# Performance work log

Measured on AMD Instinct MI355X. Metric: run time of the kernel, lower is better.

## Reference

```python
import jax, jax.numpy as jnp
import numpy as np

B, N, V, T = 16, 1024, 4096, 8


def _lsa(cost):
    """Jonker-Volgenant linear sum assignment on a square [n,n] cost matrix.
    Returns (row_ind, col_ind) minimizing cost[row, col].sum(). Equivalent to
    scipy.optimize.linear_sum_assignment for square matrices."""
    n = cost.shape[0]
    INF = np.inf
    u = np.zeros(n + 1)
    v = np.zeros(n + 1)
    p = np.zeros(n + 1, dtype=np.int64)    # p[j] = row assigned to column j (1-based)
    way = np.zeros(n + 1, dtype=np.int64)
    for i in range(1, n + 1):
        p[0] = i
        j0 = 0
        minv = np.full(n + 1, INF)
        used = np.zeros(n + 1, dtype=bool)
        while True:
            used[j0] = True
            i0 = p[j0]
            free = ~used
            free[0] = False
            cur = cost[i0 - 1, :] - u[i0] - v[1:]
            upd = free[1:] & (cur < minv[1:])
            minv[1:][upd] = cur[upd]
            way[1:][upd] = j0
            j1 = int(np.argmin(np.where(free[1:], minv[1:], INF))) + 1
            delta = minv[j1]
            u[p[used]] += delta
            v[used] -= delta
            minv[~used] -= delta
            j0 = j1
            if p[j0] == 0:
                break
        while j0:
            j1 = way[j0]
            p[j0] = p[j1]
            j0 = j1
    col_of_row = np.empty(n, dtype=np.int64)
    for j in range(1, n + 1):
        col_of_row[p[j] - 1] = j - 1
    return np.arange(n), col_of_row


def _compute_assignment(lp_np, gt_np, types_np, mask_np):
    """For each (sample, node_type) group of masked nodes, Hungarian-match
    positions to gt tokens. Returns flat (batch_idx, pos_idx, tok_idx) of all
    matched pairs. Mirrors the original type-wise padded loop (k==1 is identity)."""
    Bn = lp_np.shape[0]
    b_l, p_l, t_l = [], [], []
    for t in np.unique(types_np):
        for b in range(Bn):
            idx = np.nonzero((types_np[b] == t) & mask_np[b])[0]
            k = idx.size
            if k == 0:
                continue
            g = gt_np[b, idx]
            if k == 1:
                r = np.zeros(1, dtype=np.int64)
                c = np.zeros(1, dtype=np.int64)
            else:
                cost = -lp_np[b, idx][:, g]  # [k, k]
                r, c = _lsa(cost)
            b_l.append(np.full(k, b, dtype=np.int64))
            p_l.append(idx[r])
            t_l.append(g[c])
    return np.concatenate(b_l), np.concatenate(p_l), np.concatenate(t_l)


def setup_inputs() -> dict:
    key = jax.random.key(0)
    k1, k2, k3, k4 = jax.random.split(key, 4)
    logits = jax.random.normal(k1, (B, N, V), dtype=jnp.float32)
    gt_tokens = jax.random.randint(k2, (B, N), 0, V)
    node_types = jax.random.randint(k3, (B, N), 0, T)
    mask_positions = jax.random.randint(k4, (B, N), 0, 2).astype(bool)
    return {"logits": logits, "gt_tokens": gt_tokens,
            "node_types": node_types, "mask_positions": mask_positions}


def reference(logits, gt_tokens, node_types, mask_positions):
    # Dense log-softmax over vocab (the memory-bound bulk of the op).
    log_probs = jax.nn.log_softmax(logits, axis=-1)
    # Assignment is computed on detached values (matches .detach() in original).
    b_idx, p_idx, t_idx = _compute_assignment(
        np.asarray(jax.lax.stop_gradient(log_probs)),
        np.asarray(gt_tokens), np.asarray(node_types), np.asarray(mask_positions))
    total = b_idx.shape[0]  # total matched (masked) tokens
    sel = log_probs[jnp.asarray(b_idx), jnp.asarray(p_idx), jnp.asarray(t_idx)]
    # avg_loss = sum_b(loss_per_sample*count)/total_count == sum of matched NLL / total
    return -sel.sum() / jnp.asarray(total, sel.dtype)
```

## Files before the change

kernel.cpp:

```cpp
#include <hip/hip_runtime.h>
#include <math.h>

#define BB 16
#define NN 1024
#define VV 4096
#define TT 8
#define NG (BB*TT)
#define KMAX 124
#define STRIDE 124
#define LSEROWS 8

__device__ __forceinline__ float wave_sum(float v){
  #pragma unroll
  for (int off = 32; off; off >>= 1) v += __shfl_down(v, off);
  return v;
}

__device__ __forceinline__ unsigned fkey(float f){
  unsigned b = __float_as_uint(f);
  return b ^ ((unsigned)((int)b >> 31) | 0x80000000u);
}
__device__ __forceinline__ float inv_fkey(unsigned u){
  unsigned b = (u & 0x80000000u) ? (u ^ 0x80000000u) : ~u;
  return __uint_as_float(b);
}

__device__ __forceinline__ unsigned dpp_min64(unsigned x){
  unsigned t;
  t = (unsigned)__builtin_amdgcn_update_dpp(-1, (int)x, 0x111, 0xF, 0xF, false); x = x < t ? x : t;
  t = (unsigned)__builtin_amdgcn_update_dpp(-1, (int)x, 0x112, 0xF, 0xF, false); x = x < t ? x : t;
  t = (unsigned)__builtin_amdgcn_update_dpp(-1, (int)x, 0x114, 0xF, 0xF, false); x = x < t ? x : t;
  t = (unsigned)__builtin_amdgcn_update_dpp(-1, (int)x, 0x118, 0xF, 0xF, false); x = x < t ? x : t;
  t = (unsigned)__builtin_amdgcn_update_dpp(-1, (int)x, 0x142, 0xF, 0xF, false); x = x < t ? x : t;
  t = (unsigned)__builtin_amdgcn_update_dpp(-1, (int)x, 0x143, 0xF, 0xF, false); x = x < t ? x : t;
  return x;
}

__device__ __forceinline__ void lse_load(const float4* __restrict__ x, int lane,
                                         float4 (&v)[16]){
  #pragma unroll
  for (int i = 0; i < 16; i++) v[i] = x[lane + 64*i];
}
__device__ __forceinline__ float lse_reduce(const float4 (&v)[16]){
  float m = -INFINITY;
  #pragma unroll
  for (int i = 0; i < 16; i++)
    m = fmaxf(m, fmaxf(fmaxf(v[i].x, v[i].y), fmaxf(v[i].z, v[i].w)));
  #pragma unroll
  for (int off = 32; off; off >>= 1) m = fmaxf(m, __shfl_xor(m, off));
  float s = 0.f;
  #pragma unroll
  for (int i = 0; i < 16; i++)
    s += __expf(v[i].x - m) + __expf(v[i].y - m)
       + __expf(v[i].z - m) + __expf(v[i].w - m);
  #pragma unroll
  for (int off = 32; off; off >>= 1) s += __shfl_xor(s, off);
  return m + __logf(s);
}

__global__ __launch_bounds__(64) void k_main(const float* __restrict__ logits,
                                             const int* __restrict__ types,
                                             const int* __restrict__ gt,
                                             const unsigned char* __restrict__ raw,
                                             int* __restrict__ kcnt,
                                             float* __restrict__ gval,
                                             float* __restrict__ lse){
  int lane = threadIdx.x;

  if (blockIdx.x >= NG){
    int rbase = (blockIdx.x - NG) * LSEROWS;
    uchar4 pv = ((const uchar4*)raw)[lane];
    bool bool_layout = (__ballot((pv.y | pv.z | pv.w) != 0) != 0ull);
    const int* rawi = (const int*)raw;
    unsigned mb = 0;
    #pragma unroll
    for (int r = 0; r < LSEROWS; r++){
      int mv = bool_layout ? (int)raw[rbase + r] : rawi[rbase + r];
      mb |= (mv != 0) ? (1u << r) : 0u;
    }
    if (lane == 0){
      #pragma unroll
      for (int r = 0; r < LSEROWS; r++)
        if (!(mb & (1u << r))) lse[rbase + r] = 0.f;
    }
    if (mb == 0) return;

    float4 A[16], Bf[16];
    int rA = __ffs(mb) - 1;
    unsigned rem = mb & ~(1u << rA);
    lse_load((const float4*)(logits + (size_t)(rbase + rA) * VV), lane, A);
    while (true){
      int rB = rem ? (__ffs(rem) - 1) : -1;
      if (rB >= 0){
        rem &= ~(1u << rB);
        lse_load((const float4*)(logits + (size_t)(rbase + rB) * VV), lane, Bf);
      }
      float la = lse_reduce(A);
      if (lane == 0) lse[rbase + rA] = la;
      if (rB < 0) break;
      int rC = rem ? (__ffs(rem) - 1) : -1;
      if (rC >= 0){
        rem &= ~(1u << rC);
        lse_load((const float4*)(logits + (size_t)(rbase + rC) * VV), lane, A);
      }
      float lb = lse_reduce(Bf);
      if (lane == 0) lse[rbase + rB] = lb;
      if (rC < 0) break;
      rA = rC;
    }
    return;
  }

  __shared__ float Cm[KMAX*STRIDE];
  __shared__ float u_l[KMAX+1];
  __shared__ int   p_l[KMAX+1];
  __shared__ int   way_l[KMAX+1];
  __shared__ int   rowown[KMAX];
  __shared__ int   listA[KMAX];
  __shared__ int   listB[KMAX];
  int g = blockIdx.x, b = g >> 3, t = g & 7;
  unsigned long long lm = (1ull << lane) - 1ull;

  int local = 0;
  const uchar4* r4 = (const uchar4*)raw;
  #pragma unroll
  for (int r = 0; r < 4; r++){ uchar4 u = r4[lane + 64*r]; local |= (u.y | u.z | u.w); }
  bool bool_layout = (__ballot(local != 0) != 0ull);
  const int* rawi = (const int*)raw;
  int base = 0;
  for (int r = 0; r < NN/64; r++){
    int pos = r*64 + lane, o = b*NN + pos;
    int mv = bool_layout ? (int)raw[o] : rawi[o];
    bool pred = (types[o] == t) && (mv != 0);
    unsigned long long ball = __ballot(pred);
    int dst = base + __popcll(ball & lm);
    if (pred && dst < KMAX){ way_l[dst] = pos; listA[dst] = gt[o]; }
    base += __popcll(ball);
  }
  int k = (base > KMAX) ? KMAX : base;
  if (lane == 0) kcnt[g] = k;
  if (k == 0){ if (lane == 0) gval[g] = 0.f; return; }

  int col0 = lane + 1, col1 = lane + 65;
  bool a0 = (col0 <= k), a1 = (col1 <= k);
  int gc0 = a0 ? listA[lane]      : 0;
  int gc1 = a1 ? listA[lane + 64] : 0;

  u_l[col0] = 0.f; p_l[col0] = 0;
  if (col1 <= KMAX){ u_l[col1] = 0.f; p_l[col1] = 0; }
  if (lane == 0){ u_l[0] = 0.f; p_l[0] = 0; }
  rowown[lane] = -1;
  if (lane + 64 < KMAX) rowown[lane+64] = -1;
  __syncthreads();

  const size_t rowbase = (size_t)b * NN;
  for (int i = 0; i < k; i += 8){
    float xs0[8], xs1[8]; int rr[8];
    #pragma unroll
    for (int s = 0; s < 8; s++){
      int r = i + s; r = (r < k) ? r : (k - 1); rr[s] = r;
      const float* q = logits + (rowbase + way_l[r]) * VV;
      xs0[s] = q[gc0]; xs1[s] = q[gc1];
    }
    #pragma unroll
    for (int s = 0; s < 8; s++){
      Cm[rr[s]*STRIDE + lane]      = -xs0[s];
      Cm[rr[s]*STRIDE + 64 + lane] = -xs1[s];
    }
  }
  __syncthreads();

  float v0 = 0.f, v1 = 0.f;
  int ra0 = -1, ra1 = -1;
  if (a0){ float m = INFINITY; int rm = 0;
    for (int i = 0; i < k; i++){ float c = Cm[i*STRIDE + lane]; if (c < m){ m = c; rm = i; } }
    v0 = m; ra0 = rm; }
  if (a1){ float m = INFINITY; int rm = 0;
    for (int i = 0; i < k; i++){ float c = Cm[i*STRIDE + 64 + lane]; if (c < m){ m = c; rm = i; } }
    v1 = m; ra1 = rm; }
  if (a0){ if (atomicCAS(&rowown[ra0], -1, col0) == -1) p_l[col0] = ra0 + 1; }
  if (a1){ if (atomicCAS(&rowown[ra1], -1, col1) == -1) p_l[col1] = ra1 + 1; }
  __syncthreads();

  bool f0 = (lane < k)    && (rowown[lane]    == -1);
  bool f1 = (lane+64 < k) && (rowown[lane+64] == -1);
  unsigned long long B0 = __ballot(f0), B1 = __ballot(f1);
  int n0 = __popcll(B0);
  if (f0) listA[__popcll(B0 & lm)]      = lane + 1;
  if (f1) listA[n0 + __popcll(B1 & lm)] = lane + 65;
  int nCur = n0 + __popcll(B1);
  __syncthreads();

  int* curL = listA; int* nxtL = listB;
  for (int pass = 0; pass < 3; pass++){
    int nNxt = 0;
    for (int fr = 0; fr < nCur; fr++){
      int row = curL[fr];
      int off = (row - 1) * STRIDE;
      float rc0 = a0 ? (Cm[off + lane]      - v0) : INFINITY;
      float rc1 = a1 ? (Cm[off + 64 + lane] - v1) : INFINITY;
      unsigned k0 = fkey(rc0), k1 = fkey(rc1);
      unsigned kk = k0 < k1 ? k0 : k1;
      unsigned m1 = (unsigned)__builtin_amdgcn_readlane((int)dpp_min64(kk), 63);
      int cand = (k0 == m1) ? col0 : ((k1 == m1) ? col1 : 0);
      unsigned long long bl1 = __ballot(cand != 0);
      int ow1 = __ffsll(bl1) - 1;
      int j1 = __builtin_amdgcn_readlane(cand, ow1);
      float u1 = inv_fkey(m1);
      unsigned k0b = (col0 == j1) ? 0xFFFFFFFFu : k0;
      unsigned k1b = (col1 == j1) ? 0xFFFFFFFFu : k1;
      unsigned kkb = k0b < k1b ? k0b : k1b;
      unsigned m2 = (unsigned)__builtin_amdgcn_readlane((int)dpp_min64(kkb), 63);
      float u2 = inv_fkey(m2);
      int jt = j1;
      if (u1 < u2){
        if (col0 == j1) v0 -= (u2 - u1);
        if (col1 == j1) v1 -= (u2 - u1);
      } else {
        int own1 = p_l[j1];
        if (own1 != 0){
          int cand2 = (k0b == m2) ? col0 : ((k1b == m2) ? col1 : 0);
          unsigned long long bl2 = __ballot(cand2 != 0);
          int ow2 = __ffsll(bl2) - 1;
          jt = __builtin_amdgcn_readlane(cand2, ow2);
        }
      }
      int iprev = p_l[jt];
      if (lane == 0){ p_l[jt] = row; u_l[row] = u2; }
      if (iprev != 0){ if (lane == 0) nxtL[nNxt] = iprev; nNxt++; }
      __syncthreads();
    }
    int* tmp = curL; curL = nxtL; nxtL = tmp;
    nCur = nNxt;
  }

  for (int fr = 0; fr < nCur; fr++){
    int irow = curL[fr];
    int rp0 = a0 ? p_l[col0] : 0;
    int rp1 = a1 ? p_l[col1] : 0;
    float rpu0 = (rp0 > 0) ? u_l[rp0] : 0.f;
    float rpu1 = (rp1 > 0) ? u_l[rp1] : 0.f;
    int off = (irow - 1) * STRIDE;
    float dist0 = a0 ? (Cm[off + lane]      - v0) : INFINITY;
    float dist1 = a1 ? (Cm[off + 64 + lane] - v1) : INFINITY;
    int way0 = 0, way1 = 0;
    bool used0 = false, used1 = false;
    int j_end; float delta_end;
    while (true){
      unsigned q0 = (a0 && !used0) ? ((fkey(dist0) & 0xFFFFFF80u) | (unsigned)(col0-1)) : 0xFFFFFFFFu;
      unsigned q1 = (a1 && !used1) ? ((fkey(dist1) & 0xFFFFFF80u) | (unsigned)(col1-1)) : 0xFFFFFFFFu;
      unsigned key = q0 < q1 ? q0 : q1;
      unsigned kmin = (unsigned)__builtin_amdgcn_readlane((int)dpp_min64(key), 63);
      int j1 = (int)(kmin & 127u) + 1;
      int owner = (j1-1) & 63, slot = (j1-1) >> 6;
      float dsel  = slot ? dist1 : dist0;
      int   psel  = slot ? rp1   : rp0;
      float pusel = slot ? rpu1  : rpu0;
      float delta = __uint_as_float((unsigned)__builtin_amdgcn_readlane(__float_as_int(dsel), owner));
      int   i0    = __builtin_amdgcn_readlane(psel, owner);
      float pu    = __uint_as_float((unsigned)__builtin_amdgcn_readlane(__float_as_int(pusel), owner));
      used0 |= (j1 == col0);
      used1 |= (j1 == col1);
      if (i0 == 0){ j_end = j1; delta_end = delta; break; }
      float bse = delta - pu;
      int o2 = (i0 - 1) * STRIDE;
      float c0 = Cm[o2 + lane];
      float c1 = Cm[o2 + 64 + lane];
      float nd0 = bse + c0 - v0;
      float nd1 = bse + c1 - v1;
      if (a0 && !used0 && (nd0 < dist0)){ dist0 = nd0; way0 = j1; }
      if (a1 && !used1 && (nd1 < dist1)){ dist1 = nd1; way1 = j1; }
    }
    if (used0){ float adj = delta_end - dist0; v0 -= adj; u_l[rp0] = rpu0 + adj; }
    if (used1){ float adj = delta_end - dist1; v1 -= adj; u_l[rp1] = rpu1 + adj; }
    if (lane == 0) u_l[irow] = delta_end;
    if (a0) way_l[col0] = way0;
    if (a1) way_l[col1] = way1;
    __syncthreads();
    int j0 = j_end;
    while (true){
      int jw = way_l[j0];
      int pr = p_l[jw];
      int pw = (jw == 0) ? irow : pr;
      if (lane == 0) p_l[j0] = pw;
      if (jw == 0) break;
      j0 = jw;
    }
    __syncthreads();
  }

  __syncthreads();
  float acc = 0.f;
  if (a0) acc += Cm[(p_l[col0]-1)*STRIDE + lane];
  if (a1) acc += Cm[(p_l[col1]-1)*STRIDE + 64 + lane];
  acc = wave_sum(acc);
  if (lane == 0) gval[g] = -acc;
}

__global__ __launch_bounds__(256) void k_final(const float* __restrict__ lse,
                                               const int* __restrict__ kcnt,
                                               const float* __restrict__ gval,
                                               float* __restrict__ out){
  __shared__ double sd[256];
  __shared__ double sg[256];
  __shared__ int    si[256];
  int tid = threadIdx.x;
  double s = 0.0, gs = 0.0; int c = 0;
  for (int i = tid; i < BB*NN; i += 256) s += (double)lse[i];
  for (int i = tid; i < NG; i += 256){ gs += (double)gval[i]; c += kcnt[i]; }
  sd[tid] = s; sg[tid] = gs; si[tid] = c;
  __syncthreads();
  for (int off = 128; off; off >>= 1){
    if (tid < off){ sd[tid] += sd[tid+off]; sg[tid] += sg[tid+off]; si[tid] += si[tid+off]; }
    __syncthreads();
  }
  if (tid == 0) out[0] = (float)((sd[0] - sg[0]) / (double)si[0]);
}

extern "C" void kernel_launch(void* const* d_in, const int* in_sizes, int n_in,
                              void* d_out, int out_size, void* d_ws, size_t ws_size,
                              hipStream_t stream) {
  const float* logits = (const float*)d_in[0];
  const int*   gt     = (const int*)d_in[1];
  const int*   types  = (const int*)d_in[2];
  const unsigned char* maskraw = (const unsigned char*)d_in[3];
  float* out = (float*)d_out;

  char* w = (char*)d_ws;
  float* lse  = (float*)w;  w += (size_t)BB*NN*4;
  int*   kcnt = (int*)w;    w += 1024;
  float* gval = (float*)w;  w += 1024;

  k_main <<<NG + (BB*NN)/LSEROWS, 64, 0, stream>>>(logits, types, gt, maskraw, kcnt, gval, lse);
  k_final<<<1, 256, 0, stream>>>(lse, kcnt, gval, out);
}
```

Before: 434.3 us.

## Fuse final reduction into main kernel via atomics and interleave cost matrix as float2

```diff
diff --git a/kernel.cpp b/kernel.cpp
--- a/kernel.cpp
+++ b/kernel.cpp
@@ -7,8 +7,8 @@
 #define TT 8
 #define NG (BB*TT)
 #define KMAX 124
-#define STRIDE 124
 #define LSEROWS 8
+#define NBLK (NG + (BB*NN)/LSEROWS)
 
 __device__ __forceinline__ float wave_sum(float v){
   #pragma unroll
@@ -58,13 +58,28 @@
   return m + __logf(s);
 }
 
+__device__ __forceinline__ void finish_block(double* sd, double* sg, int* si,
+                                             unsigned* cnt, float* out, int lane){
+  if (lane != 0) return;
+  __threadfence();
+  unsigned prev = atomicAdd(cnt, 1u);
+  if (prev == (unsigned)NBLK - 1u){
+    double a = atomicAdd(sd, 0.0);
+    double b = atomicAdd(sg, 0.0);
+    int    c = atomicAdd(si, 0);
+    out[0] = (float)((a - b) / (double)c);
+  }
+}
+
 __global__ __launch_bounds__(64) void k_main(const float* __restrict__ logits,
                                              const int* __restrict__ types,
                                              const int* __restrict__ gt,
                                              const unsigned char* __restrict__ raw,
-                                             int* __restrict__ kcnt,
-                                             float* __restrict__ gval,
-                                             float* __restrict__ lse){
+                                             double* __restrict__ sd_acc,
+                                             double* __restrict__ sg_acc,
+                                             int* __restrict__ si_acc,
+                                             unsigned* __restrict__ cnt,
+                                             float* __restrict__ out){
   int lane = threadIdx.x;
 
   if (blockIdx.x >= NG){
@@ -78,13 +93,9 @@
       int mv = bool_layout ? (int)raw[rbase + r] : rawi[rbase + r];
       mb |= (mv != 0) ? (1u << r) : 0u;
     }
-    if (lane == 0){
-      #pragma unroll
-      for (int r = 0; r < LSEROWS; r++)
-        if (!(mb & (1u << r))) lse[rbase + r] = 0.f;
-    }
-    if (mb == 0) return;
-
+    if (mb == 0){ finish_block(sd_acc, sg_acc, si_acc, cnt, out, lane); return; }
+
+    double lsum = 0.0;
     float4 A[16], Bf[16];
     int rA = __ffs(mb) - 1;
     unsigned rem = mb & ~(1u << rA);
@@ -95,23 +106,23 @@
         rem &= ~(1u << rB);
         lse_load((const float4*)(logits + (size_t)(rbase + rB) * VV), lane, Bf);
       }
-      float la = lse_reduce(A);
-      if (lane == 0) lse[rbase + rA] = la;
+      lsum += (double)lse_reduce(A);
       if (rB < 0) break;
       int rC = rem ? (__ffs(rem) - 1) : -1;
       if (rC >= 0){
         rem &= ~(1u << rC);
         lse_load((const float4*)(logits + (size_t)(rbase + rC) * VV), lane, A);
       }
-      float lb = lse_reduce(Bf);
-      if (lane == 0) lse[rbase + rB] = lb;
+      lsum += (double)lse_reduce(Bf);
       if (rC < 0) break;
       rA = rC;
     }
+    if (lane == 0) atomicAdd(sd_acc, lsum);
+    finish_block(sd_acc, sg_acc, si_acc, cnt, out, lane);
     return;
   }
 
-  __shared__ float Cm[KMAX*STRIDE];
+  __shared__ float2 Cm2[KMAX*64];
   __shared__ float u_l[KMAX+1];
   __shared__ int   p_l[KMAX+1];
   __shared__ int   way_l[KMAX+1];
@@ -128,6 +139,7 @@
   bool bool_layout = (__ballot(local != 0) != 0ull);
   const int* rawi = (const int*)raw;
   int base = 0;
+  #pragma unroll
   for (int r = 0; r < NN/64; r++){
     int pos = r*64 + lane, o = b*NN + pos;
     int mv = bool_layout ? (int)raw[o] : rawi[o];
@@ -138,8 +150,10 @@
     base += __popcll(ball);
   }
   int k = (base > KMAX) ? KMAX : base;
-  if (lane == 0) kcnt[g] = k;
-  if (k == 0){ if (lane == 0) gval[g] = 0.f; return; }
+  if (k == 0){
+    finish_block(sd_acc, sg_acc, si_acc, cnt, out, lane);
+    return;
+  }
 
   int col0 = lane + 1, col1 = lane + 65;
   bool a0 = (col0 <= k), a1 = (col1 <= k);
@@ -154,30 +168,32 @@
   __syncthreads();
 
   const size_t rowbase = (size_t)b * NN;
-  for (int i = 0; i < k; i += 8){
-    float xs0[8], xs1[8]; int rr[8];
+  for (int i = 0; i < k; i += 16){
+    float xs0[16], xs1[16]; int rr[16];
     #pragma unroll
-    for (int s = 0; s < 8; s++){
+    for (int s = 0; s < 16; s++){
       int r = i + s; r = (r < k) ? r : (k - 1); rr[s] = r;
       const float* q = logits + (rowbase + way_l[r]) * VV;
       xs0[s] = q[gc0]; xs1[s] = q[gc1];
     }
     #pragma unroll
-    for (int s = 0; s < 8; s++){
-      Cm[rr[s]*STRIDE + lane]      = -xs0[s];
-      Cm[rr[s]*STRIDE + 64 + lane] = -xs1[s];
-    }
+    for (int s = 0; s < 16; s++)
+      Cm2[rr[s]*64 + lane] = make_float2(-xs0[s], -xs1[s]);
   }
   __syncthreads();
 
   float v0 = 0.f, v1 = 0.f;
   int ra0 = -1, ra1 = -1;
-  if (a0){ float m = INFINITY; int rm = 0;
-    for (int i = 0; i < k; i++){ float c = Cm[i*STRIDE + lane]; if (c < m){ m = c; rm = i; } }
-    v0 = m; ra0 = rm; }
-  if (a1){ float m = INFINITY; int rm = 0;
-    for (int i = 0; i < k; i++){ float c = Cm[i*STRIDE + 64 + lane]; if (c < m){ m = c; rm = i; } }
-    v1 = m; ra1 = rm; }
+  {
+    float m0 = INFINITY, m1 = INFINITY; int rm0 = 0, rm1 = 0;
+    for (int i = 0; i < k; i++){
+      float2 c = Cm2[i*64 + lane];
+      if (c.x < m0){ m0 = c.x; rm0 = i; }
+      if (c.y < m1){ m1 = c.y; rm1 = i; }
+    }
+    if (a0){ v0 = m0; ra0 = rm0; }
+    if (a1){ v1 = m1; ra1 = rm1; }
+  }
   if (a0){ if (atomicCAS(&rowown[ra0], -1, col0) == -1) p_l[col0] = ra0 + 1; }
   if (a1){ if (atomicCAS(&rowown[ra1], -1, col1) == -1) p_l[col1] = ra1 + 1; }
   __syncthreads();
@@ -196,9 +212,9 @@
     int nNxt = 0;
     for (int fr = 0; fr < nCur; fr++){
       int row = curL[fr];
-      int off = (row - 1) * STRIDE;
-      float rc0 = a0 ? (Cm[off + lane]      - v0) : INFINITY;
-      float rc1 = a1 ? (Cm[off + 64 + lane] - v1) : INFINITY;
+      float2 rc = Cm2[(row - 1)*64 + lane];
+      float rc0 = a0 ? (rc.x - v0) : INFINITY;
+      float rc1 = a1 ? (rc.y - v1) : INFINITY;
       unsigned k0 = fkey(rc0), k1 = fkey(rc1);
       unsigned kk = k0 < k1 ? k0 : k1;
       unsigned m1 = (unsigned)__builtin_amdgcn_readlane((int)dpp_min64(kk), 63);
@@ -228,7 +244,6 @@
       int iprev = p_l[jt];
       if (lane == 0){ p_l[jt] = row; u_l[row] = u2; }
       if (iprev != 0){ if (lane == 0) nxtL[nNxt] = iprev; nNxt++; }
-      __syncthreads();
     }
     int* tmp = curL; curL = nxtL; nxtL = tmp;
     nCur = nNxt;
@@ -240,9 +255,9 @@
     int rp1 = a1 ? p_l[col1] : 0;
     float rpu0 = (rp0 > 0) ? u_l[rp0] : 0.f;
     float rpu1 = (rp1 > 0) ? u_l[rp1] : 0.f;
-    int off = (irow - 1) * STRIDE;
-    float dist0 = a0 ? (Cm[off + lane]      - v0) : INFINITY;
-    float dist1 = a1 ? (Cm[off + 64 + lane] - v1) : INFINITY;
+    float2 dini = Cm2[(irow - 1)*64 + lane];
+    float dist0 = a0 ? (dini.x - v0) : INFINITY;
+    float dist1 = a1 ? (dini.y - v1) : INFINITY;
     int way0 = 0, way1 = 0;
     bool used0 = false, used1 = false;
     int j_end; float delta_end;
@@ -263,11 +278,9 @@
       used1 |= (j1 == col1);
       if (i0 == 0){ j_end = j1; delta_end = delta; break; }
       float bse = delta - pu;
-      int o2 = (i0 - 1) * STRIDE;
-      float c0 = Cm[o2 + lane];
-      float c1 = Cm[o2 + 64 + lane];
-      float nd0 = bse + c0 - v0;
-      float nd1 = bse + c1 - v1;
+      float2 cc = Cm2[(i0 - 1)*64 + lane];
+      float nd0 = bse + cc.x - v0;
+      float nd1 = bse + cc.y - v1;
       if (a0 && !used0 && (nd0 < dist0)){ dist0 = nd0; way0 = j1; }
       if (a1 && !used1 && (nd1 < dist1)){ dist1 = nd1; way1 = j1; }
     }
@@ -276,7 +289,6 @@
     if (lane == 0) u_l[irow] = delta_end;
     if (a0) way_l[col0] = way0;
     if (a1) way_l[col1] = way1;
-    __syncthreads();
     int j0 = j_end;
     while (true){
       int jw = way_l[j0];
@@ -286,35 +298,18 @@
       if (jw == 0) break;
       j0 = jw;
     }
-    __syncthreads();
   }
 
   __syncthreads();
   float acc = 0.f;
-  if (a0) acc += Cm[(p_l[col0]-1)*STRIDE + lane];
-  if (a1) acc += Cm[(p_l[col1]-1)*STRIDE + 64 + lane];
+  if (a0) acc += Cm2[(p_l[col0]-1)*64 + lane].x;
+  if (a1) acc += Cm2[(p_l[col1]-1)*64 + lane].y;
   acc = wave_sum(acc);
-  if (lane == 0) gval[g] = -acc;
-}
-
-__global__ __launch_bounds__(256) void k_final(const float* __restrict__ lse,
-                                               const int* __restrict__ kcnt,
-                                               const float* __restrict__ gval,
-                                               float* __restrict__ out){
-  __shared__ double sd[256];
-  __shared__ double sg[256];
-  __shared__ int    si[256];
-  int tid = threadIdx.x;
-  double s = 0.0, gs = 0.0; int c = 0;
-  for (int i = tid; i < BB*NN; i += 256) s += (double)lse[i];
-  for (int i = tid; i < NG; i += 256){ gs += (double)gval[i]; c += kcnt[i]; }
-  sd[tid] = s; sg[tid] = gs; si[tid] = c;
-  __syncthreads();
-  for (int off = 128; off; off >>= 1){
-    if (tid < off){ sd[tid] += sd[tid+off]; sg[tid] += sg[tid+off]; si[tid] += si[tid+off]; }
-    __syncthreads();
-  }
-  if (tid == 0) out[0] = (float)((sd[0] - sg[0]) / (double)si[0]);
+  if (lane == 0){
+    atomicAdd(sg_acc, (double)(-acc));
+    atomicAdd(si_acc, k);
+  }
+  finish_block(sd_acc, sg_acc, si_acc, cnt, out, lane);
 }
 
 extern "C" void kernel_launch(void* const* d_in, const int* in_sizes, int n_in,
@@ -326,11 +321,11 @@
   const unsigned char* maskraw = (const unsigned char*)d_in[3];
   float* out = (float*)d_out;
 
-  char* w = (char*)d_ws;
-  float* lse  = (float*)w;  w += (size_t)BB*NN*4;
-  int*   kcnt = (int*)w;    w += 1024;
-  float* gval = (float*)w;  w += 1024;
-
-  k_main <<<NG + (BB*NN)/LSEROWS, 64, 0, stream>>>(logits, types, gt, maskraw, kcnt, gval, lse);
-  k_final<<<1, 256, 0, stream>>>(lse, kcnt, gval, out);
-}
+  double*   sd  = (double*)d_ws;
+  double*   sg  = sd + 1;
+  int*      si  = (int*)(sg + 1);
+  unsigned* cnt = (unsigned*)(si + 1);
+  hipMemsetAsync(d_ws, 0, 32, stream);
+
+  k_main<<<NBLK, 64, 0, stream>>>(logits, types, gt, maskraw, sd, sg, si, cnt, out);
+}
```

Measured after the change: 498.1 us. +14.7%, slower.
